# Kernel optimization log

Measured on AMD Instinct MI355X. Metric: run time of the kernel, lower is better.

## Reference

```python
import jax, jax.numpy as jnp
import numpy as np

IN, H, L, B, S = 512, 1024, 6, 64, 256


def setup_inputs() -> dict:
    key = jax.random.key(0)
    ks = jax.random.split(key, 8)
    stdv = 1.0 / np.sqrt(H)
    u = lambda k, shp: jax.random.uniform(k, shp, jnp.float32, -stdv, stdv)
    x = jax.random.normal(ks[0], (B, S, IN), jnp.float32)
    # gate order along last axis of 4H: i, f, c(g), o
    U0 = u(ks[1], (IN, 4 * H))   # layer 0 input weights
    V0 = u(ks[2], (H, 4 * H))    # layer 0 recurrent weights
    b0 = u(ks[3], (4 * H,))
    U = u(ks[4], (L - 1, H, 4 * H))  # layers 1..L-1 input weights
    V = u(ks[5], (L - 1, H, 4 * H))
    b = u(ks[6], (L - 1, 4 * H))
    return {"x": x, "U0": U0, "V0": V0, "b0": b0, "U": U, "V": V, "b": b}


def _cell(xt, h, c, Um, Vm, bm):
    # fused 4-gate GEMM: [B, in] @ [in, 4H] + [B, H] @ [H, 4H]
    z = xt @ Um + h @ Vm + bm
    i, f, g, o = jnp.split(z, 4, axis=-1)
    i = jax.nn.sigmoid(i)
    f = jax.nn.sigmoid(f)
    g = jnp.tanh(g)
    o = jax.nn.sigmoid(o)
    c = f * c + i * g
    h = o * jnp.tanh(c)
    return h, c


def reference(x, U0, V0, b0, U, V, b):
    # Dropout is identity in eval mode (faithful to module.eval()).
    Bb = x.shape[0]
    h0 = jnp.zeros((L, Bb, H), x.dtype)
    c0 = jnp.zeros((L, Bb, H), x.dtype)

    def step(carry, xt):
        h, c = carry
        hs, cs = [], []
        inp = xt
        hn, cn = _cell(inp, h[0], c[0], U0, V0, b0)
        hs.append(hn); cs.append(cn); inp = hn
        for l in range(L - 1):  # fixed small layer loop
            hn, cn = _cell(inp, h[l + 1], c[l + 1], U[l], V[l], b[l])
            hs.append(hn); cs.append(cn); inp = hn
        return (jnp.stack(hs), jnp.stack(cs)), inp

    (hf, cf), seq = jax.lax.scan(step, (h0, c0), jnp.swapaxes(x, 0, 1))
    hidden_seq = jnp.swapaxes(seq, 0, 1)  # [B, S, H]
    return hidden_seq, hf, cf
```

## Files before the change

kernel.cpp:

```cpp
#include <hip/hip_runtime.h>
#include <hip/hip_cooperative_groups.h>

#define B_ 64
#define H_ 1024
#define IN_ 512
#define S_ 256
#define L_ 6
#define NG_ 4096
#define NTASK 768
#define NTICK (S_ + L_ - 1)

typedef __bf16 bf16x8 __attribute__((ext_vector_type(8)));
typedef float f32x4 __attribute__((ext_vector_type(4)));
typedef unsigned short ushort8v __attribute__((ext_vector_type(8)));
typedef unsigned short ushort_t;

#define WP_BYTES 96468992ul
#define XB_BYTES 16777216ul
#define HBF_ELEMS 786432ul
#define LSLOT 65536ul
#define XSLOT 32768ul

__host__ __device__ __forceinline__ size_t poff(int l, int jb) {
  return (l == 0) ? (size_t)jb * 49152ul
                  : 6291456ul + ((size_t)(l - 1) * 128 + jb) * 65536ul;
}

#define MFMA16(a, b, c) __builtin_amdgcn_mfma_f32_16x16x32_bf16(a, b, c, 0, 0, 0)
#define WAITN(n) asm volatile("s_waitcnt vmcnt(" #n ")" ::: "memory")

__device__ __forceinline__ unsigned short f2bf(float f) {
  union { float f; unsigned u; } v; v.f = f;
  unsigned r = v.u + 0x7fffu + ((v.u >> 16) & 1u);
  return (unsigned short)(r >> 16);
}

__global__ void k_pack_w(const float* __restrict__ U0, const float* __restrict__ V0,
                         const float* __restrict__ U, const float* __restrict__ V,
                         ushort_t* __restrict__ Wp) {
  const int bx = blockIdx.x;
  const int l = bx >> 7, jb = bx & 127;
  ushort_t* __restrict__ panel = Wp + poff(l, jb);
  const int KU = (l == 0) ? IN_ : H_;
  const int NU = KU >> 6;
  const int NCH = NU + 16;
  const float* __restrict__ Usrc = (l == 0) ? U0 : U + (size_t)(l - 1) * H_ * NG_;
  const float* __restrict__ Vsrc = (l == 0) ? V0 : V + (size_t)(l - 1) * H_ * NG_;
  const int t = threadIdx.x, lane = t & 63, g4 = t >> 6;
  const int l15 = lane & 15, kg = lane >> 4;
  for (int p = 0; p < NCH; ++p) {
    const int gi = p * 4 + g4;
    const int c = gi >> 2, u = gi & 3, nf = u >> 1, ks = u & 1;
    const int n = (nf * 2 + (l15 >> 3)) * 1024 + jb * 8 + (l15 & 7);
    const int k = c * 64 + ks * 32 + kg * 8;
    const float* __restrict__ src =
        (c < NU) ? (Usrc + (size_t)k * NG_ + n)
                 : (Vsrc + (size_t)(k - KU) * NG_ + n);
    ushort8v uv;
#pragma unroll
    for (int e = 0; e < 8; ++e) uv[e] = f2bf(src[(size_t)e * NG_]);
    *(ushort8v*)(panel + (size_t)gi * 512 + lane * 8) = uv;
  }
}

__global__ void k_cvt_x(const float* __restrict__ x, ushort_t* __restrict__ xb) {
  const int tt = blockIdx.x;
  const int tid = threadIdx.x;
  const int b = tid >> 2, kq = (tid & 3) << 7;
  const float* __restrict__ src = x + ((size_t)b * S_ + tt) * IN_ + kq;
  ushort_t* __restrict__ dst = xb + (size_t)tt * XSLOT;
  const int w = b >> 4, l15 = b & 15;
#pragma unroll
  for (int kk = 0; kk < 128; kk += 8) {
    float4 v0 = *(const float4*)(src + kk);
    float4 v1 = *(const float4*)(src + kk + 4);
    ushort8v u = { f2bf(v0.x), f2bf(v0.y), f2bf(v0.z), f2bf(v0.w),
                   f2bf(v1.x), f2bf(v1.y), f2bf(v1.z), f2bf(v1.w) };
    const int k = kq + kk;
    const int ks = k >> 5, kg = (k & 31) >> 3;
    *(ushort8v*)(dst + (((size_t)ks * 4 + w) * 64 + kg * 16 + l15) * 8) = u;
  }
}

template<int NCH>
__device__ __forceinline__ void gemm_tick(f32x4 acc[2],
                                          const ushort_t* __restrict__ panel,
                                          const ushort_t* __restrict__ A1,
                                          const ushort_t* __restrict__ A2,
                                          int w, int lane) {
  constexpr int NU = NCH - 16;
  bf16x8 Wb[4][4];
  bf16x8 Ab[4][2];
#define LDU(p) (*(const bf16x8*)(p))
#define ISSUE(c) do { \
    const ushort_t* wp_ = panel + (size_t)(c) * 2048 + lane * 8; \
    Wb[(c) & 3][0] = LDU(wp_); \
    Wb[(c) & 3][1] = LDU(wp_ + 512); \
    Wb[(c) & 3][2] = LDU(wp_ + 1024); \
    Wb[(c) & 3][3] = LDU(wp_ + 1536); \
    const ushort_t* ap_ = ((c) < NU \
        ? A1 + ((size_t)(2 * (c)) * 4 + w) * 512 \
        : A2 + ((size_t)(2 * ((c) - NU)) * 4 + w) * 512) + lane * 8; \
    Ab[(c) & 3][0] = LDU(ap_); \
    Ab[(c) & 3][1] = LDU(ap_ + 2048); \
  } while (0)
  ISSUE(0); ISSUE(1); ISSUE(2);
#pragma unroll
  for (int c = 0; c < NCH; ++c) {
    if (c + 3 < NCH) ISSUE(c + 3);
    const int rem = NCH - 1 - c;
    if (rem >= 3) { WAITN(18); }
    else if (rem == 2) { WAITN(12); }
    else if (rem == 1) { WAITN(6); }
    else { WAITN(0); }
    acc[0] = MFMA16(Ab[c & 3][0], Wb[c & 3][0], acc[0]);
    acc[1] = MFMA16(Ab[c & 3][0], Wb[c & 3][2], acc[1]);
    acc[0] = MFMA16(Ab[c & 3][1], Wb[c & 3][1], acc[0]);
    acc[1] = MFMA16(Ab[c & 3][1], Wb[c & 3][3], acc[1]);
  }
#undef ISSUE
#undef LDU
}

__global__ void __launch_bounds__(256, 2)
k_lstm(const ushort_t* __restrict__ xb,
       const ushort_t* __restrict__ Wp,
       const float* __restrict__ b0,
       const float* __restrict__ bL,
       ushort_t* __restrict__ hbf,
       float* __restrict__ out, int multi) {
  cooperative_groups::grid_group grid = cooperative_groups::this_grid();
  float* __restrict__ seq = out;
  float* __restrict__ hf = out + (size_t)B_ * S_ * H_;
  float* __restrict__ cf = hf + (size_t)L_ * B_ * H_;
  __shared__ float hstF[512];

  const int tid = threadIdx.x;
  const int w = tid >> 6;
  const int lane = tid & 63;
  const int l15 = lane & 15;
  const int kg = lane >> 4;
  const bool lo = (l15 < 8);
  const int wg = blockIdx.x;
  const int nwg = gridDim.x;

  float creg[4] = {0.f, 0.f, 0.f, 0.f};

  for (int T = 0; T < NTICK; ++T) {
    for (int task = wg; task < NTASK; task += nwg) {
      const int l = task >> 7;
      const int jb = task & 127;
      const int t = T - l;
      if (t < 0 || t >= S_) continue;
      const ushort_t* __restrict__ hprev = hbf + (size_t)((T + 1) & 1) * (L_ * LSLOT);
      ushort_t* __restrict__ hcur = hbf + (size_t)(T & 1) * (L_ * LSLOT);
      const ushort_t* __restrict__ panel = Wp + poff(l, jb);
      const ushort_t* __restrict__ A2 = hprev + (size_t)l * LSLOT;

      f32x4 acc[2];
      acc[0] = (f32x4){0.f, 0.f, 0.f, 0.f};
      acc[1] = (f32x4){0.f, 0.f, 0.f, 0.f};
      if (l == 0)
        gemm_tick<24>(acc, panel, xb + (size_t)t * XSLOT, A2, w, lane);
      else
        gemm_tick<32>(acc, panel, hprev + (size_t)(l - 1) * LSLOT, A2, w, lane);

      const int hc = (jb << 3) + (l15 & 7);
      const float* __restrict__ bias = (l == 0) ? b0 : (bL + (size_t)(l - 1) * NG_);
      const float bi = bias[hc];
      const float bfv = bias[1024 + hc];
      const float bgv = bias[2048 + hc];
      const float bov = bias[3072 + hc];

#pragma unroll
      for (int j = 0; j < 4; ++j) {
        float a0 = acc[0][j], a1 = acc[1][j];
        float p0 = __shfl_xor(a0, 8, 64);
        float p1 = __shfl_xor(a1, 8, 64);
        float zi = (lo ? a0 : p0) + bi;
        float zf = (lo ? p0 : a0) + bfv;
        float zg = (lo ? a1 : p1) + bgv;
        float zo = (lo ? p1 : a1) + bov;
        float iv = 1.f / (1.f + expf(-zi));
        float fv = 1.f / (1.f + expf(-zf));
        float gv = tanhf(zg);
        float ov = 1.f / (1.f + expf(-zo));
        const int r = w * 16 + kg * 4 + j;
        float cold;
        if (multi)
          cold = (t > 0) ? cf[((size_t)l * B_ + r) * H_ + hc] : 0.f;
        else
          cold = creg[j];
        float cn = fv * cold + iv * gv;
        creg[j] = cn;
        float hv = ov * tanhf(cn);
        if (lo) {
          hstF[w * 128 + (kg * 4 + j) * 8 + l15] = hv;
          if (multi || t == S_ - 1) cf[((size_t)l * B_ + r) * H_ + hc] = cn;
          if (t == S_ - 1) hf[((size_t)l * B_ + r) * H_ + hc] = hv;
        }
      }
      __syncthreads();
      if (kg == 0) {
        const int lr = l15;
        float4 v0 = *(const float4*)&hstF[w * 128 + lr * 8];
        float4 v1 = *(const float4*)&hstF[w * 128 + lr * 8 + 4];
        ushort8v u8 = { f2bf(v0.x), f2bf(v0.y), f2bf(v0.z), f2bf(v0.w),
                        f2bf(v1.x), f2bf(v1.y), f2bf(v1.z), f2bf(v1.w) };
        *(ushort8v*)(hcur + (size_t)l * LSLOT +
                     (((size_t)(jb >> 2) * 4 + w) * 64 + (jb & 3) * 16 + lr) * 8) = u8;
        if (l == L_ - 1) {
          float* sp = seq + (((size_t)(w * 16 + lr)) * S_ + t) * H_ + (jb << 3);
          *(float4*)sp = v0;
          *(float4*)(sp + 4) = v1;
        }
      }
      __syncthreads();
    }
    grid.sync();
  }
}

extern "C" void kernel_launch(void* const* d_in, const int* in_sizes, int n_in,
                              void* d_out, int out_size, void* d_ws, size_t ws_size,
                              hipStream_t stream) {
  const float* x = (const float*)d_in[0];
  const float* U0 = (const float*)d_in[1];
  const float* V0 = (const float*)d_in[2];
  const float* b0 = (const float*)d_in[3];
  const float* U = (const float*)d_in[4];
  const float* V = (const float*)d_in[5];
  const float* bL = (const float*)d_in[6];
  float* out = (float*)d_out;

  char* ws = (char*)d_ws;
  unsigned short* Wp = (unsigned short*)ws;
  unsigned short* xb = (unsigned short*)(ws + WP_BYTES);
  unsigned short* hbf = (unsigned short*)(ws + WP_BYTES + XB_BYTES);

  hipLaunchKernelGGL(k_pack_w, dim3(NTASK), dim3(256), 0, stream, U0, V0, U, V, Wp);
  hipLaunchKernelGGL(k_cvt_x, dim3(S_), dim3(256), 0, stream, x, xb);
  hipMemsetAsync(hbf, 0, HBF_ELEMS * 2, stream);

  int maxB = 0;
  hipOccupancyMaxActiveBlocksPerMultiprocessor(&maxB, k_lstm, 256, 0);
  int nwg = maxB * 256;
  if (nwg > NTASK) nwg = NTASK;
  if (nwg < 64) nwg = 64;
  int multi = (nwg < NTASK) ? 1 : 0;

  void* args[] = { (void*)&xb, (void*)&Wp, (void*)&b0, (void*)&bL,
                   (void*)&hbf, (void*)&out, (void*)&multi };
  hipError_t e = hipLaunchCooperativeKernel((void*)k_lstm, dim3(nwg), dim3(256),
                                            args, 0, stream);
  if (e != hipSuccess) {
    (void)hipGetLastError();
    nwg = 256; multi = 1;
    void* args2[] = { (void*)&xb, (void*)&Wp, (void*)&b0, (void*)&bL,
                      (void*)&hbf, (void*)&out, (void*)&multi };
    hipLaunchCooperativeKernel((void*)k_lstm, dim3(nwg), dim3(256),
                               args2, 0, stream);
  }
}
```

Measured before the change: 16.84 ms.

## Rewrite LSTM as persistent weight-stationary kernel with split-K producer/consumer workgroups

Replaces the task-loop LSTM kernel with 192 persistent 1024-thread workgroups. Each workgroup holds its slice of the packed weights in registers for the whole sequence, streams activations through an LDS ring via global_load_lds, and splits K between a U-half and a V-half workgroup. The two halves exchange bf16 partial sums through a global buffer guarded by release/acquire flags, which removes the per-tick reload of the whole weight matrix. In exchange it adds bf16 rounding of the partial sums, flag spin-waits, and a hard dependency on all 192 large workgroups being co-resident.

```diff
diff --git a/kernel.cpp b/kernel.cpp
--- a/kernel.cpp
+++ b/kernel.cpp
@@ -7,7 +7,7 @@
 #define S_ 256
 #define L_ 6
 #define NG_ 4096
-#define NTASK 768
+#define NWG 192
 #define NTICK (S_ + L_ - 1)
 
 typedef __bf16 bf16x8 __attribute__((ext_vector_type(8)));
@@ -17,7 +17,10 @@
 
 #define WP_BYTES 96468992ul
 #define XB_BYTES 16777216ul
-#define HBF_ELEMS 786432ul
+#define HBF_BYTES 1572864ul
+#define BIASP_BYTES 98304ul
+#define FLAGS_BYTES 1024ul
+#define ZU_BYTES 3145728ul
 #define LSLOT 65536ul
 #define XSLOT 32768ul
 
@@ -33,6 +36,14 @@
   union { float f; unsigned u; } v; v.f = f;
   unsigned r = v.u + 0x7fffu + ((v.u >> 16) & 1u);
   return (unsigned short)(r >> 16);
+}
+__device__ __forceinline__ float bfbits2f(unsigned short u) {
+  union { unsigned u32; float f; } v; v.u32 = ((unsigned)u) << 16; return v.f;
+}
+__device__ __forceinline__ void gload_lds(const ushort_t* g, ushort_t* l) {
+  __builtin_amdgcn_global_load_lds(
+      (const __attribute__((address_space(1))) unsigned int*)g,
+      (__attribute__((address_space(3))) unsigned int*)l, 16, 0, 0);
 }
 
 __global__ void k_pack_w(const float* __restrict__ U0, const float* __restrict__ V0,
@@ -66,158 +77,203 @@
 __global__ void k_cvt_x(const float* __restrict__ x, ushort_t* __restrict__ xb) {
   const int tt = blockIdx.x;
   const int tid = threadIdx.x;
-  const int b = tid >> 2, kq = (tid & 3) << 7;
-  const float* __restrict__ src = x + ((size_t)b * S_ + tt) * IN_ + kq;
+  const int ln = tid & 63, grp = tid >> 6;
   ushort_t* __restrict__ dst = xb + (size_t)tt * XSLOT;
-  const int w = b >> 4, l15 = b & 15;
-#pragma unroll
-  for (int kk = 0; kk < 128; kk += 8) {
-    float4 v0 = *(const float4*)(src + kk);
-    float4 v1 = *(const float4*)(src + kk + 4);
-    ushort8v u = { f2bf(v0.x), f2bf(v0.y), f2bf(v0.z), f2bf(v0.w),
-                   f2bf(v1.x), f2bf(v1.y), f2bf(v1.z), f2bf(v1.w) };
-    const int k = kq + kk;
-    const int ks = k >> 5, kg = (k & 31) >> 3;
-    *(ushort8v*)(dst + (((size_t)ks * 4 + w) * 64 + kg * 16 + l15) * 8) = u;
-  }
-}
-
-template<int NCH>
-__device__ __forceinline__ void gemm_tick(f32x4 acc[2],
-                                          const ushort_t* __restrict__ panel,
-                                          const ushort_t* __restrict__ A1,
-                                          const ushort_t* __restrict__ A2,
-                                          int w, int lane) {
-  constexpr int NU = NCH - 16;
-  bf16x8 Wb[4][4];
-  bf16x8 Ab[4][2];
-#define LDU(p) (*(const bf16x8*)(p))
-#define ISSUE(c) do { \
-    const ushort_t* wp_ = panel + (size_t)(c) * 2048 + lane * 8; \
-    Wb[(c) & 3][0] = LDU(wp_); \
-    Wb[(c) & 3][1] = LDU(wp_ + 512); \
-    Wb[(c) & 3][2] = LDU(wp_ + 1024); \
-    Wb[(c) & 3][3] = LDU(wp_ + 1536); \
-    const ushort_t* ap_ = ((c) < NU \
-        ? A1 + ((size_t)(2 * (c)) * 4 + w) * 512 \
-        : A2 + ((size_t)(2 * ((c) - NU)) * 4 + w) * 512) + lane * 8; \
-    Ab[(c) & 3][0] = LDU(ap_); \
-    Ab[(c) & 3][1] = LDU(ap_ + 2048); \
-  } while (0)
-  ISSUE(0); ISSUE(1); ISSUE(2);
-#pragma unroll
-  for (int c = 0; c < NCH; ++c) {
-    if (c + 3 < NCH) ISSUE(c + 3);
-    const int rem = NCH - 1 - c;
-    if (rem >= 3) { WAITN(18); }
-    else if (rem == 2) { WAITN(12); }
-    else if (rem == 1) { WAITN(6); }
-    else { WAITN(0); }
-    acc[0] = MFMA16(Ab[c & 3][0], Wb[c & 3][0], acc[0]);
-    acc[1] = MFMA16(Ab[c & 3][0], Wb[c & 3][2], acc[1]);
-    acc[0] = MFMA16(Ab[c & 3][1], Wb[c & 3][1], acc[0]);
-    acc[1] = MFMA16(Ab[c & 3][1], Wb[c & 3][3], acc[1]);
-  }
-#undef ISSUE
-#undef LDU
-}
-
-__global__ void __launch_bounds__(256, 2)
-k_lstm(const ushort_t* __restrict__ xb,
-       const ushort_t* __restrict__ Wp,
-       const float* __restrict__ b0,
-       const float* __restrict__ bL,
-       ushort_t* __restrict__ hbf,
-       float* __restrict__ out, int multi) {
-  cooperative_groups::grid_group grid = cooperative_groups::this_grid();
+  for (int u = grp; u < 64; u += 4) {
+    const int c = u >> 3, ks = (u & 7) >> 2, m = u & 3;
+    const int row = m * 16 + (ln & 15);
+    const int k = c * 64 + ks * 32 + (ln >> 4) * 8;
+    const float* __restrict__ src = x + ((size_t)row * S_ + tt) * IN_ + k;
+    float4 v0 = *(const float4*)(src);
+    float4 v1 = *(const float4*)(src + 4);
+    ushort8v uv = { f2bf(v0.x), f2bf(v0.y), f2bf(v0.z), f2bf(v0.w),
+                    f2bf(v1.x), f2bf(v1.y), f2bf(v1.z), f2bf(v1.w) };
+    *(ushort8v*)(dst + (size_t)u * 512 + ln * 8) = uv;
+  }
+}
+
+__global__ void k_pack_bias(const float* __restrict__ b0, const float* __restrict__ bL,
+                            float* __restrict__ biasp) {
+  int i = blockIdx.x * 256 + threadIdx.x;
+  if (i < 6144) {
+    int l = i >> 10, h = i & 1023;
+    const float* src = (l == 0) ? b0 : bL + (size_t)(l - 1) * NG_;
+#pragma unroll
+    for (int g = 0; g < 4; ++g) biasp[(size_t)i * 4 + g] = src[g * 1024 + h];
+  }
+}
+
+template<int NC, bool ISV>
+__device__ __forceinline__ void body(
+    cooperative_groups::grid_group& grid, int l, int cg, int coff,
+    const ushort_t* __restrict__ xb, const ushort_t* __restrict__ Wp,
+    const float* __restrict__ biasp, ushort_t* __restrict__ hbf,
+    int* __restrict__ flags, ushort_t* __restrict__ zu,
+    float* __restrict__ out, ushort_t* ring, ushort_t* hst) {
   float* __restrict__ seq = out;
   float* __restrict__ hf = out + (size_t)B_ * S_ * H_;
   float* __restrict__ cf = hf + (size_t)L_ * B_ * H_;
-  __shared__ float hstF[512];
+  ushort_t* zlds = ring;
 
   const int tid = threadIdx.x;
-  const int w = tid >> 6;
-  const int lane = tid & 63;
-  const int l15 = lane & 15;
-  const int kg = lane >> 4;
-  const bool lo = (l15 < 8);
-  const int wg = blockIdx.x;
-  const int nwg = gridDim.x;
-
+  const int wv = tid >> 6, lane = tid & 63;
+  const int l15 = lane & 15, kg = lane >> 4;
+  const int gp = wv >> 3, hs = wv & 7;
+  const int jb = cg * 8 + hs;
+
+  bf16x8 Wreg[NC][2];
+  {
+    const ushort_t* pb = Wp + poff(l, jb) + (size_t)coff * 2048;
+#pragma unroll
+    for (int c = 0; c < NC; ++c)
+#pragma unroll
+      for (int ks = 0; ks < 2; ++ks)
+        Wreg[c][ks] = *(const bf16x8*)(pb + (size_t)(c * 4 + gp * 2 + ks) * 512 + lane * 8);
+  }
+
+  const int fr = tid >> 4;
+  const int fh0 = (tid & 15) << 2;
   float creg[4] = {0.f, 0.f, 0.f, 0.f};
+  f32x4 breg[4];
+  if (ISV) {
+#pragma unroll
+    for (int q = 0; q < 4; ++q)
+      breg[q] = *(const f32x4*)(biasp + ((size_t)l * 1024 + cg * 64 + fh0 + q) * 4);
+  }
+  const int fidx = l * 16 + cg;
+  constexpr int NCH2 = NC / 2;
 
   for (int T = 0; T < NTICK; ++T) {
-    for (int task = wg; task < NTASK; task += nwg) {
-      const int l = task >> 7;
-      const int jb = task & 127;
-      const int t = T - l;
-      if (t < 0 || t >= S_) continue;
-      const ushort_t* __restrict__ hprev = hbf + (size_t)((T + 1) & 1) * (L_ * LSLOT);
-      ushort_t* __restrict__ hcur = hbf + (size_t)(T & 1) * (L_ * LSLOT);
-      const ushort_t* __restrict__ panel = Wp + poff(l, jb);
-      const ushort_t* __restrict__ A2 = hprev + (size_t)l * LSLOT;
-
-      f32x4 acc[2];
-      acc[0] = (f32x4){0.f, 0.f, 0.f, 0.f};
-      acc[1] = (f32x4){0.f, 0.f, 0.f, 0.f};
-      if (l == 0)
-        gemm_tick<24>(acc, panel, xb + (size_t)t * XSLOT, A2, w, lane);
-      else
-        gemm_tick<32>(acc, panel, hprev + (size_t)(l - 1) * LSLOT, A2, w, lane);
-
-      const int hc = (jb << 3) + (l15 & 7);
-      const float* __restrict__ bias = (l == 0) ? b0 : (bL + (size_t)(l - 1) * NG_);
-      const float bi = bias[hc];
-      const float bfv = bias[1024 + hc];
-      const float bgv = bias[2048 + hc];
-      const float bov = bias[3072 + hc];
-
-#pragma unroll
-      for (int j = 0; j < 4; ++j) {
-        float a0 = acc[0][j], a1 = acc[1][j];
-        float p0 = __shfl_xor(a0, 8, 64);
-        float p1 = __shfl_xor(a1, 8, 64);
-        float zi = (lo ? a0 : p0) + bi;
-        float zf = (lo ? p0 : a0) + bfv;
-        float zg = (lo ? a1 : p1) + bgv;
-        float zo = (lo ? p1 : a1) + bov;
-        float iv = 1.f / (1.f + expf(-zi));
-        float fv = 1.f / (1.f + expf(-zf));
-        float gv = tanhf(zg);
-        float ov = 1.f / (1.f + expf(-zo));
-        const int r = w * 16 + kg * 4 + j;
-        float cold;
-        if (multi)
-          cold = (t > 0) ? cf[((size_t)l * B_ + r) * H_ + hc] : 0.f;
-        else
-          cold = creg[j];
-        float cn = fv * cold + iv * gv;
-        creg[j] = cn;
-        float hv = ov * tanhf(cn);
-        if (lo) {
-          hstF[w * 128 + (kg * 4 + j) * 8 + l15] = hv;
-          if (multi || t == S_ - 1) cf[((size_t)l * B_ + r) * H_ + hc] = cn;
-          if (t == S_ - 1) hf[((size_t)l * B_ + r) * H_ + hc] = hv;
+    const int t = T - l;
+    if (t >= 0 && t < S_) {
+      const ushort_t* Ab;
+      if (!ISV && l == 0) Ab = xb + (size_t)t * XSLOT;
+      else {
+        const int lA = ISV ? l : (l - 1);
+        Ab = hbf + (size_t)((T + 1) & 1) * (L_ * LSLOT) + (size_t)lA * LSLOT;
+      }
+      ushort_t* hcur = hbf + (size_t)(T & 1) * (L_ * LSLOT) + (size_t)l * LSLOT;
+
+      f32x4 acc[4];
+#pragma unroll
+      for (int m = 0; m < 4; ++m) acc[m] = (f32x4){0.f, 0.f, 0.f, 0.f};
+
+#define STAGE(j) gload_lds(Ab + (size_t)(j) * 8192 + wv * 512 + lane * 8, \
+                           ring + ((j) % 3) * 8192 + wv * 512)
+      STAGE(0); STAGE(1);
+#pragma unroll
+      for (int j = 0; j < NCH2; ++j) {
+        if (j + 1 < NCH2) { WAITN(1); } else { WAITN(0); }
+        __builtin_amdgcn_s_barrier();
+        if (j + 2 < NCH2) STAGE(j + 2);
+        const ushort_t* rb = ring + (j % 3) * 8192;
+#pragma unroll
+        for (int cc = 0; cc < 2; ++cc)
+#pragma unroll
+          for (int ks = 0; ks < 2; ++ks) {
+            const int base = (cc * 8 + ks * 4) * 512 + lane * 8;
+            bf16x8 A0 = *(const bf16x8*)(rb + base);
+            bf16x8 A1 = *(const bf16x8*)(rb + base + 512);
+            bf16x8 A2 = *(const bf16x8*)(rb + base + 1024);
+            bf16x8 A3 = *(const bf16x8*)(rb + base + 1536);
+            acc[0] = MFMA16(A0, Wreg[j * 2 + cc][ks], acc[0]);
+            acc[1] = MFMA16(A1, Wreg[j * 2 + cc][ks], acc[1]);
+            acc[2] = MFMA16(A2, Wreg[j * 2 + cc][ks], acc[2]);
+            acc[3] = MFMA16(A3, Wreg[j * 2 + cc][ks], acc[3]);
+          }
+      }
+#undef STAGE
+      __syncthreads();
+#pragma unroll
+      for (int m = 0; m < 4; ++m)
+#pragma unroll
+        for (int jj = 0; jj < 4; ++jj)
+          zlds[wv * 1024 + (m * 16 + kg * 4 + jj) * 16 + l15] = f2bf(acc[m][jj]);
+      __syncthreads();
+
+      ushort_t* slot = zu + (size_t)fidx * 16384;
+      if (!ISV) {
+#pragma unroll
+        for (int q = 0; q < 4; ++q) {
+          const int hcl = fh0 + q;
+          const int fb = (hcl >> 3) * 1024 + fr * 16 + (hcl & 7);
+          unsigned v01 = (unsigned)zlds[fb] | ((unsigned)zlds[fb + 8] << 16);
+          unsigned v23 = (unsigned)zlds[8 * 1024 + fb] | ((unsigned)zlds[8 * 1024 + fb + 8] << 16);
+          *(uint2*)(slot + ((size_t)fr * 64 + hcl) * 4) = make_uint2(v01, v23);
+        }
+        __threadfence();
+        __syncthreads();
+        if (tid == 0)
+          __hip_atomic_store(&flags[fidx], t + 1, __ATOMIC_RELEASE, __HIP_MEMORY_SCOPE_AGENT);
+      } else {
+        if (tid == 0) {
+          while (__hip_atomic_load(&flags[fidx], __ATOMIC_ACQUIRE,
+                                   __HIP_MEMORY_SCOPE_AGENT) < t + 1)
+            __builtin_amdgcn_s_sleep(2);
+        }
+        __syncthreads();
+#pragma unroll
+        for (int q = 0; q < 4; ++q) {
+          const int hcl = fh0 + q;
+          const int fb = (hcl >> 3) * 1024 + fr * 16 + (hcl & 7);
+          float zv0 = bfbits2f(zlds[fb]);
+          float zv1 = bfbits2f(zlds[fb + 8]);
+          float zv2 = bfbits2f(zlds[8 * 1024 + fb]);
+          float zv3 = bfbits2f(zlds[8 * 1024 + fb + 8]);
+          unsigned long long up = __hip_atomic_load(
+              (const unsigned long long*)(slot + ((size_t)fr * 64 + hcl) * 4),
+              __ATOMIC_RELAXED, __HIP_MEMORY_SCOPE_AGENT);
+          float zi = zv0 + bfbits2f((unsigned short)up) + breg[q][0];
+          float zf = zv1 + bfbits2f((unsigned short)(up >> 16)) + breg[q][1];
+          float zg = zv2 + bfbits2f((unsigned short)(up >> 32)) + breg[q][2];
+          float zo = zv3 + bfbits2f((unsigned short)(up >> 48)) + breg[q][3];
+          float iv = 1.f / (1.f + expf(-zi));
+          float fv = 1.f / (1.f + expf(-zf));
+          float gv = tanhf(zg);
+          float ov = 1.f / (1.f + expf(-zo));
+          float cn = fv * creg[q] + iv * gv;
+          creg[q] = cn;
+          float hv = ov * tanhf(cn);
+          hst[fr * 64 + hcl] = f2bf(hv);
+          const int hc = cg * 64 + hcl;
+          if (l == L_ - 1) seq[((size_t)fr * S_ + t) * H_ + hc] = hv;
+          if (t == S_ - 1) {
+            cf[((size_t)l * B_ + fr) * H_ + hc] = cn;
+            hf[((size_t)l * B_ + fr) * H_ + hc] = hv;
+          }
+        }
+        __syncthreads();
+        if (tid < 512) {
+          const int u = tid >> 6, ln = tid & 63;
+          const int m = u & 3, ks = u >> 2;
+          ushort8v v = *(const ushort8v*)(hst + (m * 16 + (ln & 15)) * 64 +
+                                          ks * 32 + (ln >> 4) * 8);
+          *(ushort8v*)(hcur + ((size_t)cg * 8 + u) * 512 + ln * 8) = v;
         }
       }
-      __syncthreads();
-      if (kg == 0) {
-        const int lr = l15;
-        float4 v0 = *(const float4*)&hstF[w * 128 + lr * 8];
-        float4 v1 = *(const float4*)&hstF[w * 128 + lr * 8 + 4];
-        ushort8v u8 = { f2bf(v0.x), f2bf(v0.y), f2bf(v0.z), f2bf(v0.w),
-                        f2bf(v1.x), f2bf(v1.y), f2bf(v1.z), f2bf(v1.w) };
-        *(ushort8v*)(hcur + (size_t)l * LSLOT +
-                     (((size_t)(jb >> 2) * 4 + w) * 64 + (jb & 3) * 16 + lr) * 8) = u8;
-        if (l == L_ - 1) {
-          float* sp = seq + (((size_t)(w * 16 + lr)) * S_ + t) * H_ + (jb << 3);
-          *(float4*)sp = v0;
-          *(float4*)(sp + 4) = v1;
-        }
-      }
-      __syncthreads();
     }
     grid.sync();
+  }
+}
+
+__global__ void __launch_bounds__(1024, 1)
+k_lstm(const ushort_t* __restrict__ xb, const ushort_t* __restrict__ Wp,
+       const float* __restrict__ biasp, ushort_t* __restrict__ hbf,
+       int* __restrict__ flags, ushort_t* __restrict__ zu,
+       float* __restrict__ out) {
+  cooperative_groups::grid_group grid = cooperative_groups::this_grid();
+  __shared__ __align__(16) ushort_t ring[3 * 8192];
+  __shared__ __align__(16) ushort_t hst[4096];
+  const int wg = blockIdx.x;
+  const int l = wg >> 5, rr = wg & 31, role = rr >> 4, cg = rr & 15;
+  if (role == 0) {
+    if (l == 0)
+      body<8, false>(grid, l, cg, 0, xb, Wp, biasp, hbf, flags, zu, out, ring, hst);
+    else
+      body<16, false>(grid, l, cg, 0, xb, Wp, biasp, hbf, flags, zu, out, ring, hst);
+  } else {
+    body<16, true>(grid, l, cg, (l == 0) ? 8 : 16, xb, Wp, biasp, hbf, flags, zu, out,
+                   ring, hst);
   }
 }
 
@@ -237,28 +293,18 @@
   unsigned short* Wp = (unsigned short*)ws;
   unsigned short* xb = (unsigned short*)(ws + WP_BYTES);
   unsigned short* hbf = (unsigned short*)(ws + WP_BYTES + XB_BYTES);
-
-  hipLaunchKernelGGL(k_pack_w, dim3(NTASK), dim3(256), 0, stream, U0, V0, U, V, Wp);
+  float* biasp = (float*)(ws + WP_BYTES + XB_BYTES + HBF_BYTES);
+  int* flags = (int*)(ws + WP_BYTES + XB_BYTES + HBF_BYTES + BIASP_BYTES);
+  unsigned short* zu = (unsigned short*)(ws + WP_BYTES + XB_BYTES + HBF_BYTES +
+                                         BIASP_BYTES + FLAGS_BYTES);
+
+  hipLaunchKernelGGL(k_pack_w, dim3(768), dim3(256), 0, stream, U0, V0, U, V, Wp);
   hipLaunchKernelGGL(k_cvt_x, dim3(S_), dim3(256), 0, stream, x, xb);
-  hipMemsetAsync(hbf, 0, HBF_ELEMS * 2, stream);
-
-  int maxB = 0;
-  hipOccupancyMaxActiveBlocksPerMultiprocessor(&maxB, k_lstm, 256, 0);
-  int nwg = maxB * 256;
-  if (nwg > NTASK) nwg = NTASK;
-  if (nwg < 64) nwg = 64;
-  int multi = (nwg < NTASK) ? 1 : 0;
-
-  void* args[] = { (void*)&xb, (void*)&Wp, (void*)&b0, (void*)&bL,
-                   (void*)&hbf, (void*)&out, (void*)&multi };
-  hipError_t e = hipLaunchCooperativeKernel((void*)k_lstm, dim3(nwg), dim3(256),
-                                            args, 0, stream);
-  if (e != hipSuccess) {
-    (void)hipGetLastError();
-    nwg = 256; multi = 1;
-    void* args2[] = { (void*)&xb, (void*)&Wp, (void*)&b0, (void*)&bL,
-                      (void*)&hbf, (void*)&out, (void*)&multi };
-    hipLaunchCooperativeKernel((void*)k_lstm, dim3(nwg), dim3(256),
-                               args2, 0, stream);
-  }
-}
+  hipLaunchKernelGGL(k_pack_bias, dim3(24), dim3(256), 0, stream, b0, bL, biasp);
+  hipMemsetAsync(hbf, 0, HBF_BYTES, stream);
+  hipMemsetAsync(flags, 0, FLAGS_BYTES, stream);
+
+  void* args[] = { (void*)&xb, (void*)&Wp, (void*)&biasp, (void*)&hbf,
+                   (void*)&flags, (void*)&zu, (void*)&out };
+  hipLaunchCooperativeKernel((void*)k_lstm, dim3(NWG), dim3(1024), args, 0, stream);
+}
```

Result: slower. 24.63 ms (+46.2%).
